# Performance work log

Measured on AMD Instinct MI355X. Metric: run time of the kernel, lower is better.

## Reference

```python
import jax, jax.numpy as jnp
import numpy as np

B, S, HID = 1, 2048, 4096
NH, NKV, HD = 32, 8, 128
GROUPS = NH // NKV
SCALING = HD ** -0.5


def approx_matmul(a, b):
    # BaselineApproxMatmulFP16: matmul performed in fp16 precision
    return jnp.matmul(a.astype(jnp.float16), b.astype(jnp.float16)).astype(a.dtype)


def rotate_half(x):
    x1, x2 = jnp.split(x, 2, axis=-1)
    return jnp.concatenate([-x2, x1], axis=-1)


def setup_inputs() -> dict:
    key = jax.random.key(0)
    ks = jax.random.split(key, 6)
    hidden_states = jax.random.normal(ks[0], (B, S, HID), jnp.float32)
    # Proper RoPE tables (HF llama convention: freqs duplicated across halves)
    inv_freq = 1.0 / (10000.0 ** (jnp.arange(0, HD, 2, dtype=jnp.float32) / HD))
    t = jnp.arange(S, dtype=jnp.float32)
    freqs = jnp.outer(t, inv_freq)                      # [S, HD/2]
    emb = jnp.concatenate([freqs, freqs], axis=-1)      # [S, HD]
    cos = jnp.cos(emb)[None]                            # [B, S, HD]
    sin = jnp.sin(emb)[None]
    # Additive causal mask [B,1,S,S]
    causal = jnp.triu(jnp.full((S, S), -1e9, jnp.float32), k=1)[None, None]
    scale = 0.02
    wq = jax.random.normal(ks[1], (HID, NH * HD), jnp.float32) * scale
    wk = jax.random.normal(ks[2], (HID, NKV * HD), jnp.float32) * scale
    wv = jax.random.normal(ks[3], (HID, NKV * HD), jnp.float32) * scale
    wo = jax.random.normal(ks[4], (NH * HD, HID), jnp.float32) * scale
    return {"hidden_states": hidden_states, "cos": cos, "sin": sin,
            "attn_mask": causal, "wq": wq, "wk": wk, "wv": wv, "wo": wo}


def reference(hidden_states, cos, sin, attn_mask, wq, wk, wv, wo):
    x = hidden_states
    # projections -> [B, heads, S, HD]
    q = (x @ wq).reshape(B, S, NH, HD).transpose(0, 2, 1, 3)
    k = (x @ wk).reshape(B, S, NKV, HD).transpose(0, 2, 1, 3)
    v = (x @ wv).reshape(B, S, NKV, HD).transpose(0, 2, 1, 3)
    # RoPE
    c = cos[:, None]  # [B,1,S,HD]
    s = sin[:, None]
    q = q * c + rotate_half(q) * s
    k = k * c + rotate_half(k) * s
    # repeat_kv (GQA): [B,NKV,S,HD] -> [B,NH,S,HD]
    k = jnp.repeat(k, GROUPS, axis=1)
    v = jnp.repeat(v, GROUPS, axis=1)
    # eager attention with fp16 approx matmul
    attn = approx_matmul(q, k.transpose(0, 1, 3, 2)) * SCALING  # [B,NH,S,S]
    attn = attn + attn_mask
    attn = jax.nn.softmax(attn.astype(jnp.float32), axis=-1).astype(q.dtype)
    out = approx_matmul(attn, v)                                # [B,NH,S,HD]
    out = out.transpose(0, 2, 1, 3).reshape(B, S, NH * HD)
    return out @ wo
```

## Files before the change

### kernel.cpp

```cpp
#include <hip/hip_runtime.h>
#include <hip/hip_bf16.h>
#include <hip/hip_fp16.h>

typedef _Float16 half8 __attribute__((ext_vector_type(8)));
typedef _Float16 half4 __attribute__((ext_vector_type(4)));
typedef float f32x4 __attribute__((ext_vector_type(4)));
typedef unsigned int u32;

#define S_LEN 2048
#define HID_DIM 4096
#define N_HEADS 32
#define N_KV 8
#define HEAD_DIM 128
#define SCALE_QK 0.08838834764831845f

__device__ __forceinline__ void async16(void* lds, const void* gptr) {
  __builtin_amdgcn_global_load_lds(
      (const __attribute__((address_space(1))) u32*)gptr,
      (__attribute__((address_space(3))) u32*)lds, 16, 0, 0);
}

__global__ void conv_f32_f16(const float* __restrict__ src, _Float16* __restrict__ dst, int n8) {
  int i = blockIdx.x * 256 + threadIdx.x;
  if (i < n8) {
    float4 a = ((const float4*)src)[2 * i];
    float4 b = ((const float4*)src)[2 * i + 1];
    half8 h;
    h[0] = (_Float16)a.x; h[1] = (_Float16)a.y; h[2] = (_Float16)a.z; h[3] = (_Float16)a.w;
    h[4] = (_Float16)b.x; h[5] = (_Float16)b.y; h[6] = (_Float16)b.z; h[7] = (_Float16)b.w;
    ((half8*)dst)[i] = h;
  }
}

__global__ void transpose_f32_f16(const float* __restrict__ src, _Float16* __restrict__ dst,
                                  int R, int C) {
  __shared__ float tile[64][73];
  const int t = threadIdx.x;
  const int bx = blockIdx.x;
  const int by = blockIdx.y;
  {
    const int c4 = (t & 15) * 4;
    const int r0 = t >> 4;
#pragma unroll
    for (int i = 0; i < 4; i++) {
      int r = r0 + 16 * i;
      float4 v = *(const float4*)&src[(long)(by * 64 + r) * C + bx * 64 + c4];
      tile[r][c4] = v.x; tile[r][c4 + 1] = v.y; tile[r][c4 + 2] = v.z; tile[r][c4 + 3] = v.w;
    }
  }
  __syncthreads();
  const int kc = t & 7;
  const int n0 = t >> 3;
#pragma unroll
  for (int p = 0; p < 2; p++) {
    int n = n0 + 32 * p;
    half8 o;
#pragma unroll
    for (int j = 0; j < 8; j++) o[j] = (_Float16)tile[kc * 8 + j][n];
    *(half8*)&dst[(long)(bx * 64 + n) * R + by * 64 + kc * 8] = o;
  }
}

template <int NHEADS>
__global__ void rope_tiled(_Float16* __restrict__ t, const float* __restrict__ cosb,
                           const float* __restrict__ sinb) {
  int idx = blockIdx.x * 256 + threadIdx.x;
  int slo = idx & 15;
  int d8 = (idx >> 4) & 7;
  int h = (idx >> 7) % NHEADS;
  int s16 = idx / (128 * NHEADS);
  int s = s16 * 16 + slo;
  int d0 = d8 * 8;
  long c0 = (long)(h * 128 + s16) * 4;
  long base = (c0 + (d0 >> 5)) * 512 + ((d0 >> 3) & 3) * 128 + slo * 8;
  half8 a = *(half8*)(t + base);
  half8 b = *(half8*)(t + base + 1024);
  const float* cp = cosb + s * 128 + d0;
  const float* sp = sinb + s * 128 + d0;
  half8 olo, ohi;
#pragma unroll
  for (int j = 0; j < 8; j++) {
    float c = cp[j], sn = sp[j];
    float av = (float)a[j], bv = (float)b[j];
    olo[j] = (_Float16)(av * c - bv * sn);
    ohi[j] = (_Float16)(bv * c + av * sn);
  }
  *(half8*)(t + base) = olo;
  *(half8*)(t + base + 1024) = ohi;
}

__global__ __launch_bounds__(256, 3) void gemm_qkv(
    const _Float16* __restrict__ A, const _Float16* __restrict__ BtQ,
    const _Float16* __restrict__ BtKV, _Float16* __restrict__ Qt,
    _Float16* __restrict__ Kt, _Float16* __restrict__ Vt) {
  __shared__ _Float16 As[128 * 64];
  __shared__ _Float16 Bs[128 * 64];
  const int K = 4096;
  const int tid = threadIdx.x, lane = tid & 63, wid = tid >> 6;
  const int row0 = blockIdx.y * 128;
  const int col0 = blockIdx.x * 128;
  const int wm = wid >> 1, wn = wid & 1;
  const int lr = lane & 15, lg = lane >> 4;

  const _Float16* bbase = (col0 < 4096) ? (BtQ + (long)col0 * K)
                                        : (BtKV + (long)(col0 - 4096) * K);
  const int scol = ((lane & 7) ^ ((lane >> 3) & 7)) * 8;
  const _Float16* aptr = A + (long)(row0 + wid * 32 + (lane >> 3)) * K + scol;
  const _Float16* bptr = bbase + (long)(wid * 32 + (lane >> 3)) * K + scol;
  _Float16* alds = As + (wid * 4) * 512;
  _Float16* blds = Bs + (wid * 4) * 512;

  f32x4 acc[4][4] = {};
  for (int k0 = 0; k0 < K; k0 += 64) {
#pragma unroll
    for (int j = 0; j < 4; j++) {
      async16(alds + j * 512, aptr + k0 + (long)j * 8 * K);
      async16(blds + j * 512, bptr + k0 + (long)j * 8 * K);
    }
    __syncthreads();
    half8 a[2][4], b[2][4];
#pragma unroll
    for (int kk = 0; kk < 2; kk++)
#pragma unroll
      for (int mf = 0; mf < 4; mf++) {
        a[kk][mf] = *(const half8*)&As[(wm * 64 + mf * 16 + lr) * 64 +
                                       (((kk * 4 + lg) ^ (lr & 7)) * 8)];
        b[kk][mf] = *(const half8*)&Bs[(wn * 64 + mf * 16 + lr) * 64 +
                                       (((kk * 4 + lg) ^ (lr & 7)) * 8)];
      }
#pragma unroll
    for (int kk = 0; kk < 2; kk++)
#pragma unroll
      for (int mf = 0; mf < 4; mf++)
#pragma unroll
        for (int nf = 0; nf < 4; nf++)
          acc[mf][nf] =
              __builtin_amdgcn_mfma_f32_16x16x32_f16(a[kk][mf], b[kk][nf], acc[mf][nf], 0, 0, 0);
    __syncthreads();
  }

#pragma unroll
  for (int mf = 0; mf < 4; mf++) {
#pragma unroll
    for (int nf = 0; nf < 4; nf++) {
      int rbase = row0 + wm * 64 + mf * 16 + lg * 4;
      int col = col0 + wn * 64 + nf * 16 + lr;
      if (col0 < 4096) {
        int h = col >> 7, d = col & 127;
        long off = ((long)((h * 128 + (rbase >> 4)) * 4 + (d >> 5))) * 512 +
                   ((d >> 3) & 3) * 128 + (rbase & 15) * 8 + (d & 7);
#pragma unroll
        for (int i = 0; i < 4; i++) Qt[off + i * 8] = (_Float16)acc[mf][nf][i];
      } else if (col0 < 5120) {
        int gc = col - 4096;
        int g = gc >> 7, d = gc & 127;
        long off = ((long)((g * 128 + (rbase >> 4)) * 4 + (d >> 5))) * 512 +
                   ((d >> 3) & 3) * 128 + (rbase & 15) * 8 + (d & 7);
#pragma unroll
        for (int i = 0; i < 4; i++) Kt[off + i * 8] = (_Float16)acc[mf][nf][i];
      } else {
        int gc = col - 5120;
        int gq = gc >> 7, d = gc & 127;
        int dt = d >> 4, lrr = d & 15;
        int kvb = rbase >> 5, lgv = (rbase >> 3) & 3, j = rbase & 7;
        half4 v;
#pragma unroll
        for (int i = 0; i < 4; i++) v[i] = (_Float16)acc[mf][nf][i];
        long off = ((long)(gq * 64 + kvb) * 8 + dt) * 512 + (lgv * 16 + lrr) * 8 + j;
        *(half4*)&Vt[off] = v;
      }
    }
  }
}

__global__ __launch_bounds__(256, 3) void gemm_out(
    const _Float16* __restrict__ A, const _Float16* __restrict__ Bt,
    float* __restrict__ C) {
  __shared__ _Float16 As[128 * 64];
  __shared__ _Float16 Bs[128 * 64];
  const int K = 4096;
  const int tid = threadIdx.x, lane = tid & 63, wid = tid >> 6;
  const int row0 = blockIdx.y * 128;
  const int col0 = blockIdx.x * 128;
  const int wm = wid >> 1, wn = wid & 1;
  const int lr = lane & 15, lg = lane >> 4;

  const int scol = ((lane & 7) ^ ((lane >> 3) & 7)) * 8;
  const _Float16* aptr = A + (long)(row0 + wid * 32 + (lane >> 3)) * K + scol;
  const _Float16* bptr = Bt + (long)(col0 + wid * 32 + (lane >> 3)) * K + scol;
  _Float16* alds = As + (wid * 4) * 512;
  _Float16* blds = Bs + (wid * 4) * 512;

  f32x4 acc[4][4] = {};
  for (int k0 = 0; k0 < K; k0 += 64) {
#pragma unroll
    for (int j = 0; j < 4; j++) {
      async16(alds + j * 512, aptr + k0 + (long)j * 8 * K);
      async16(blds + j * 512, bptr + k0 + (long)j * 8 * K);
    }
    __syncthreads();
    half8 a[2][4], b[2][4];
#pragma unroll
    for (int kk = 0; kk < 2; kk++)
#pragma unroll
      for (int mf = 0; mf < 4; mf++) {
        a[kk][mf] = *(const half8*)&As[(wm * 64 + mf * 16 + lr) * 64 +
                                       (((kk * 4 + lg) ^ (lr & 7)) * 8)];
        b[kk][mf] = *(const half8*)&Bs[(wn * 64 + mf * 16 + lr) * 64 +
                                       (((kk * 4 + lg) ^ (lr & 7)) * 8)];
      }
#pragma unroll
    for (int kk = 0; kk < 2; kk++)
#pragma unroll
      for (int mf = 0; mf < 4; mf++)
#pragma unroll
        for (int nf = 0; nf < 4; nf++)
          acc[mf][nf] =
              __builtin_amdgcn_mfma_f32_16x16x32_f16(a[kk][mf], b[kk][nf], acc[mf][nf], 0, 0, 0);
    __syncthreads();
  }
#pragma unroll
  for (int mf = 0; mf < 4; mf++)
#pragma unroll
    for (int nf = 0; nf < 4; nf++) {
      int rbase = row0 + wm * 64 + mf * 16 + lg * 4;
      int col = col0 + wn * 64 + nf * 16 + lr;
#pragma unroll
      for (int i = 0; i < 4; i++)
        C[(long)(rbase + i) * 4096 + col] = acc[mf][nf][i];
    }
}

__global__ __launch_bounds__(256, 3) void attn_kernel(
    const _Float16* __restrict__ Qt, const _Float16* __restrict__ Kt,
    const _Float16* __restrict__ Vt, _Float16* __restrict__ O,
    const float* __restrict__ cosb, const float* __restrict__ sinb) {
  __shared__ _Float16 Klds[2][4096];
  __shared__ _Float16 Vlds[2][4096];
  __shared__ _Float16 P_lds[4][512];
  const int tid = threadIdx.x;
  const int lane = tid & 63;
  const int wid = tid >> 6;
  const int bid = blockIdx.x;
  const int g = bid & 7;
  const int qidx = bid >> 3;
  const int qt16 = (qidx < 64) ? (2 * qidx) : (2 * (127 - qidx) + 1);
  const int h = g * 4 + wid;
  const int qrow0 = qt16 * 16;
  const int ntiles = (qrow0 + 47) >> 5;
  const int lr = lane & 15;
  const int lg = lane >> 4;

  half8 qf[4];
  {
    const _Float16* qp = Qt + ((long)(h * 128 + qt16) * 4) * 512 + lane * 8;
#pragma unroll
    for (int t = 0; t < 4; t++) qf[t] = *(const half8*)(qp + t * 512);
    int s = qrow0 + lr;
#pragma unroll
    for (int t = 0; t < 2; t++) {
      const float* cp = cosb + s * 128 + t * 32 + lg * 8;
      const float* sp = sinb + s * 128 + t * 32 + lg * 8;
#pragma unroll
      for (int j = 0; j < 8; j++) {
        float c = cp[j], sn = sp[j];
        float lo = (float)qf[t][j], hi = (float)qf[t + 2][j];
        qf[t][j]     = (_Float16)(lo * c - hi * sn);
        qf[t + 2][j] = (_Float16)(hi * c + lo * sn);
      }
    }
  }

  const _Float16* kgb = Kt + (long)g * 128 * 2048 + lane * 8;
  const _Float16* vgb = Vt + (long)g * 64 * 4096 + lane * 8;

  {
    async16(&Klds[0][(2 * wid) * 512], kgb + (2 * wid) * 512);
    async16(&Klds[0][(2 * wid + 1) * 512], kgb + (2 * wid + 1) * 512);
    async16(&Vlds[0][(2 * wid) * 512], vgb + (2 * wid) * 512);
    async16(&Vlds[0][(2 * wid + 1) * 512], vgb + (2 * wid + 1) * 512);
  }
  __syncthreads();

  f32x4 oacc[8] = {};
  float mrow[4] = {-1e30f, -1e30f, -1e30f, -1e30f};
  float lsum[4] = {0.f, 0.f, 0.f, 0.f};

  for (int t = 0; t < ntiles; t++) {
    const int kb = t * 32;
    const int cur = t & 1;
    if (t + 1 < ntiles) {
      const _Float16* ks = kgb + (long)(t + 1) * 4096;
      const _Float16* vs = vgb + (long)(t + 1) * 4096;
      async16(&Klds[cur ^ 1][(2 * wid) * 512], ks + (2 * wid) * 512);
      async16(&Klds[cur ^ 1][(2 * wid + 1) * 512], ks + (2 * wid + 1) * 512);
      async16(&Vlds[cur ^ 1][(2 * wid) * 512], vs + (2 * wid) * 512);
      async16(&Vlds[cur ^ 1][(2 * wid + 1) * 512], vs + (2 * wid + 1) * 512);
    }

    half8 kf[8];
#pragma unroll
    for (int c = 0; c < 8; c++)
      kf[c] = *(const half8*)&Klds[cur][c * 512 + lane * 8];
    half8 vf[8];
#pragma unroll
    for (int dt = 0; dt < 8; dt++)
      vf[dt] = *(const half8*)&Vlds[cur][dt * 512 + lane * 8];

    f32x4 sacc[2] = {};
#pragma unroll
    for (int s = 0; s < 2; s++)
#pragma unroll
      for (int t2 = 0; t2 < 4; t2++)
        sacc[s] = __builtin_amdgcn_mfma_f32_16x16x32_f16(qf[t2], kf[s * 4 + t2], sacc[s], 0, 0, 0);

    float mx[4];
    bool grow = false;
#pragma unroll
    for (int i = 0; i < 4; i++) {
      int qrow = qrow0 + lg * 4 + i;
      float s0 = sacc[0][i] * SCALE_QK;
      float s1 = sacc[1][i] * SCALE_QK;
      if (kb + lr > qrow) s0 = -1e30f;
      if (kb + 16 + lr > qrow) s1 = -1e30f;
      sacc[0][i] = s0; sacc[1][i] = s1;
      mx[i] = fmaxf(s0, s1);
      grow |= (mx[i] > mrow[i] + 4.0f);
    }
    if (__any((int)grow)) {
#pragma unroll
      for (int i = 0; i < 4; i++) {
        float m = mx[i];
        m = fmaxf(m, __shfl_xor(m, 1));
        m = fmaxf(m, __shfl_xor(m, 2));
        m = fmaxf(m, __shfl_xor(m, 4));
        m = fmaxf(m, __shfl_xor(m, 8));
        float mn = fmaxf(mrow[i], m);
        float scl = __expf(mrow[i] - mn);
        mrow[i] = mn;
        lsum[i] *= scl;
#pragma unroll
        for (int dt = 0; dt < 8; dt++) oacc[dt][i] *= scl;
      }
    }
    float p[2][4];
#pragma unroll
    for (int i = 0; i < 4; i++) {
      p[0][i] = __expf(sacc[0][i] - mrow[i]);
      p[1][i] = __expf(sacc[1][i] - mrow[i]);
      lsum[i] += p[0][i] + p[1][i];
    }

#pragma unroll
    for (int sub = 0; sub < 2; sub++)
#pragma unroll
      for (int i = 0; i < 4; i++)
        P_lds[wid][(lg * 4 + i) * 32 + sub * 16 + lr] = (_Float16)p[sub][i];
    half8 pa = *(const half8*)&P_lds[wid][lr * 32 + lg * 8];

#pragma unroll
    for (int dt = 0; dt < 8; dt++)
      oacc[dt] = __builtin_amdgcn_mfma_f32_16x16x32_f16(pa, vf[dt], oacc[dt], 0, 0, 0);

    __syncthreads();
  }

#pragma unroll
  for (int i = 0; i < 4; i++) {
    float t2 = lsum[i];
    t2 += __shfl_xor(t2, 1);
    t2 += __shfl_xor(t2, 2);
    t2 += __shfl_xor(t2, 4);
    t2 += __shfl_xor(t2, 8);
    lsum[i] = t2;
  }
#pragma unroll
  for (int dt = 0; dt < 8; dt++) {
#pragma unroll
    for (int i = 0; i < 4; i++) {
      float o = oacc[dt][i] / lsum[i];
      O[(long)(qrow0 + lg * 4 + i) * HID_DIM + h * HEAD_DIM + dt * 16 + lr] = (_Float16)o;
    }
  }
}

extern "C" void kernel_launch(void* const* d_in, const int* in_sizes, int n_in,
                              void* d_out, int out_size, void* d_ws, size_t ws_size,
                              hipStream_t stream) {
  const float* x    = (const float*)d_in[0];
  const float* cosb = (const float*)d_in[1];
  const float* sinb = (const float*)d_in[2];
  const float* wq = (const float*)d_in[4];
  const float* wk = (const float*)d_in[5];
  const float* wv = (const float*)d_in[6];
  const float* wo = (const float*)d_in[7];
  float* out = (float*)d_out;

  char* ws = (char*)d_ws;
  _Float16* Xh    = (_Float16*)(ws);
  _Float16* Oattn = Xh;
  _Float16* Qt    = (_Float16*)(ws + (size_t)(16 << 20));
  _Float16* Kt    = (_Float16*)(ws + (size_t)(32 << 20));
  _Float16* Vt    = (_Float16*)(ws + (size_t)(36 << 20));
  _Float16* WqT   = (_Float16*)(ws + (size_t)(40 << 20));
  _Float16* WoT   = WqT;
  _Float16* WkvT  = (_Float16*)d_out;

  dim3 b256(256);

  conv_f32_f16<<<dim3(S_LEN * HID_DIM / 8 / 256), b256, 0, stream>>>(x, Xh, S_LEN * HID_DIM / 8);

  transpose_f32_f16<<<dim3(4096 / 64, 4096 / 64), b256, 0, stream>>>(wq, WqT, 4096, 4096);
  transpose_f32_f16<<<dim3(1024 / 64, 4096 / 64), b256, 0, stream>>>(wk, WkvT, 4096, 1024);
  transpose_f32_f16<<<dim3(1024 / 64, 4096 / 64), b256, 0, stream>>>(wv, WkvT + (size_t)1024 * 4096, 4096, 1024);

  gemm_qkv<<<dim3(6144 / 128, S_LEN / 128), b256, 0, stream>>>(Xh, WqT, WkvT, Qt, Kt, Vt);

  rope_tiled<N_KV><<<dim3(N_KV * 16384 / 256), b256, 0, stream>>>(Kt, cosb, sinb);

  attn_kernel<<<dim3(1024), b256, 0, stream>>>(Qt, Kt, Vt, Oattn, cosb, sinb);

  transpose_f32_f16<<<dim3(4096 / 64, 4096 / 64), b256, 0, stream>>>(wo, WoT, 4096, 4096);
  gemm_out<<<dim3(4096 / 128, S_LEN / 128), b256, 0, stream>>>(Oattn, WoT, out);
}
```

Measured before the change: 320.1 us.

## Merge input conversion and weight transposes into one prep kernel; raise MFMA priority

Replaces the separate fp32-to-fp16 conversion launch and three weight-transpose launches with a single prep kernel that dispatches on block index. This removes three kernel launches and the tail gaps between them. It also wraps the QK and PV MFMA sequences in the attention kernel with s_setprio(1)/s_setprio(0) so waves issuing matrix instructions are favored by the scheduler. The prep kernel now allocates the transpose LDS tile even for conversion blocks, which may lower occupancy for that part of the work.

Result: no change. 317.1 us (-0.9%).

```diff
diff --git a/kernel.cpp b/kernel.cpp
--- a/kernel.cpp
+++ b/kernel.cpp
@@ -20,24 +20,9 @@
       (__attribute__((address_space(3))) u32*)lds, 16, 0, 0);
 }
 
-__global__ void conv_f32_f16(const float* __restrict__ src, _Float16* __restrict__ dst, int n8) {
-  int i = blockIdx.x * 256 + threadIdx.x;
-  if (i < n8) {
-    float4 a = ((const float4*)src)[2 * i];
-    float4 b = ((const float4*)src)[2 * i + 1];
-    half8 h;
-    h[0] = (_Float16)a.x; h[1] = (_Float16)a.y; h[2] = (_Float16)a.z; h[3] = (_Float16)a.w;
-    h[4] = (_Float16)b.x; h[5] = (_Float16)b.y; h[6] = (_Float16)b.z; h[7] = (_Float16)b.w;
-    ((half8*)dst)[i] = h;
-  }
-}
-
-__global__ void transpose_f32_f16(const float* __restrict__ src, _Float16* __restrict__ dst,
-                                  int R, int C) {
-  __shared__ float tile[64][73];
-  const int t = threadIdx.x;
-  const int bx = blockIdx.x;
-  const int by = blockIdx.y;
+__device__ __forceinline__ void transpose_tile(const float* __restrict__ src,
+                                               _Float16* __restrict__ dst, int R, int C,
+                                               int bx, int by, float (*tile)[73], int t) {
   {
     const int c4 = (t & 15) * 4;
     const int r0 = t >> 4;
@@ -59,6 +44,39 @@
     for (int j = 0; j < 8; j++) o[j] = (_Float16)tile[kc * 8 + j][n];
     *(half8*)&dst[(long)(bx * 64 + n) * R + by * 64 + kc * 8] = o;
   }
+}
+
+__global__ void prep_kernel(const float* __restrict__ x, _Float16* __restrict__ Xh,
+                            const float* __restrict__ wq, _Float16* __restrict__ WqT,
+                            const float* __restrict__ wk, const float* __restrict__ wv,
+                            _Float16* __restrict__ WkvT) {
+  __shared__ float tile[64][73];
+  const int bid = blockIdx.x;
+  const int t = threadIdx.x;
+  if (bid < 4096) {
+    int i = bid * 256 + t;
+    float4 a = ((const float4*)x)[2 * i];
+    float4 b = ((const float4*)x)[2 * i + 1];
+    half8 h;
+    h[0] = (_Float16)a.x; h[1] = (_Float16)a.y; h[2] = (_Float16)a.z; h[3] = (_Float16)a.w;
+    h[4] = (_Float16)b.x; h[5] = (_Float16)b.y; h[6] = (_Float16)b.z; h[7] = (_Float16)b.w;
+    ((half8*)Xh)[i] = h;
+  } else if (bid < 8192) {
+    int tt = bid - 4096;
+    transpose_tile(wq, WqT, 4096, 4096, tt & 63, tt >> 6, tile, t);
+  } else if (bid < 9216) {
+    int tt = bid - 8192;
+    transpose_tile(wk, WkvT, 4096, 1024, tt & 15, tt >> 4, tile, t);
+  } else {
+    int tt = bid - 9216;
+    transpose_tile(wv, WkvT + (size_t)1024 * 4096, 4096, 1024, tt & 15, tt >> 4, tile, t);
+  }
+}
+
+__global__ void transpose_f32_f16(const float* __restrict__ src, _Float16* __restrict__ dst,
+                                  int R, int C) {
+  __shared__ float tile[64][73];
+  transpose_tile(src, dst, R, C, blockIdx.x, blockIdx.y, tile, threadIdx.x);
 }
 
 template <int NHEADS>
@@ -308,11 +326,13 @@
       vf[dt] = *(const half8*)&Vlds[cur][dt * 512 + lane * 8];
 
     f32x4 sacc[2] = {};
+    __builtin_amdgcn_s_setprio(1);
 #pragma unroll
     for (int s = 0; s < 2; s++)
 #pragma unroll
       for (int t2 = 0; t2 < 4; t2++)
         sacc[s] = __builtin_amdgcn_mfma_f32_16x16x32_f16(qf[t2], kf[s * 4 + t2], sacc[s], 0, 0, 0);
+    __builtin_amdgcn_s_setprio(0);
 
     float mx[4];
     bool grow = false;
@@ -358,9 +378,11 @@
         P_lds[wid][(lg * 4 + i) * 32 + sub * 16 + lr] = (_Float16)p[sub][i];
     half8 pa = *(const half8*)&P_lds[wid][lr * 32 + lg * 8];
 
+    __builtin_amdgcn_s_setprio(1);
 #pragma unroll
     for (int dt = 0; dt < 8; dt++)
       oacc[dt] = __builtin_amdgcn_mfma_f32_16x16x32_f16(pa, vf[dt], oacc[dt], 0, 0, 0);
+    __builtin_amdgcn_s_setprio(0);
 
     __syncthreads();
   }
@@ -408,11 +430,7 @@
 
   dim3 b256(256);
 
-  conv_f32_f16<<<dim3(S_LEN * HID_DIM / 8 / 256), b256, 0, stream>>>(x, Xh, S_LEN * HID_DIM / 8);
-
-  transpose_f32_f16<<<dim3(4096 / 64, 4096 / 64), b256, 0, stream>>>(wq, WqT, 4096, 4096);
-  transpose_f32_f16<<<dim3(1024 / 64, 4096 / 64), b256, 0, stream>>>(wk, WkvT, 4096, 1024);
-  transpose_f32_f16<<<dim3(1024 / 64, 4096 / 64), b256, 0, stream>>>(wv, WkvT + (size_t)1024 * 4096, 4096, 1024);
+  prep_kernel<<<dim3(10240), b256, 0, stream>>>(x, Xh, wq, WqT, wk, wv, WkvT);
 
   gemm_qkv<<<dim3(6144 / 128, S_LEN / 128), b256, 0, stream>>>(Xh, WqT, WkvT, Qt, Kt, Vt);
 
```
